# Kernel optimization log

Measured on AMD Instinct MI355X. Metric: run time of the kernel, lower is better.

The kernel has to match this reference:

```python
import jax, jax.numpy as jnp
import numpy as np

B, L, D = 32, 2048, 768
H = 512
EPS = 1e-5  # batch_norm eps (PyG MLP default norm)


def setup_inputs() -> dict:
    key = jax.random.key(0)
    ks = jax.random.split(key, 8)
    hidden = jax.random.normal(ks[0], (B, L, D), dtype=jnp.float32)
    attention_mask = jax.random.randint(ks[1], (B, L), 0, 2, dtype=jnp.int32)
    W1 = jax.random.normal(ks[2], (D, H), dtype=jnp.float32) * 0.02
    b1 = jnp.zeros((H,), dtype=jnp.float32)
    gamma = jnp.ones((H,), dtype=jnp.float32)
    beta = jnp.zeros((H,), dtype=jnp.float32)
    W2 = jax.random.normal(ks[3], (H, H), dtype=jnp.float32) * 0.02
    b2 = jnp.zeros((H,), dtype=jnp.float32)
    return {"hidden": hidden, "attention_mask": attention_mask,
            "W1": W1, "b1": b1, "gamma": gamma, "beta": beta,
            "W2": W2, "b2": b2}


def reference(hidden, attention_mask, W1, b1, gamma, beta, W2, b2):
    # Valid-token mask; pads are excluded from the batched graph's node set.
    m = attention_mask.astype(hidden.dtype)[..., None]  # (B, L, 1)
    n_valid = jnp.maximum(jnp.sum(m), 1.0)

    # MLP layer 1: Linear -> BatchNorm (stats over all valid nodes across the
    # whole batched graph, mirroring PyG MLP training-mode batch_norm) -> ReLU
    h = jnp.einsum('bld,dh->blh', hidden, W1) + b1  # (B, L, H)
    mean = jnp.sum(h * m, axis=(0, 1)) / n_valid
    var = jnp.sum(jnp.square(h - mean) * m, axis=(0, 1)) / n_valid
    h = (h - mean) * jax.lax.rsqrt(var + EPS) * gamma + beta
    h = jax.nn.relu(h)

    # MLP layer 2 (plain_last: no norm/act)
    out = jnp.einsum('blh,hk->blk', h, W2) + b2  # (B, L, H)

    # scores == ones -> segment softmax over each sequence's valid tokens is
    # uniform 1/n_b; scatter_add over batch ids == masked mean pool.
    counts = jnp.maximum(jnp.sum(m, axis=1), 1.0)  # (B, 1)
    pooled = jnp.sum(out * m, axis=1) / counts  # (B, H)
    return pooled
```

## Files before the change

### kernel.cpp

```cpp
#include <hip/hip_runtime.h>
#include <hip/hip_bf16.h>

#define Bn 32
#define Ln 2048
#define Dn 768
#define Hn 512
#define Mn (Bn*Ln)
#define EPSC 1e-5f

#define OFF_S1   0
#define OFF_S2   512
#define OFF_CNT  2048
#define OFF_PH   2304
#define OFF_W1T_BYTES  131072
#define OFF_H_BYTES    1048576

#define BM 128
#define BN2 256
#define BK 64
#define LDK 72

typedef __attribute__((ext_vector_type(8))) short bf16x8;
typedef __attribute__((ext_vector_type(4))) float f32x4;

static __device__ __forceinline__ unsigned short f2bf(float x) {
  __hip_bfloat16 h = __float2bfloat16(x);
  return *reinterpret_cast<unsigned short*>(&h);
}
static __device__ __forceinline__ float bf2f(unsigned short u) {
  return __uint_as_float(((unsigned int)u) << 16);
}

__global__ __launch_bounds__(256) void pre_kernel(const int* __restrict__ mask,
                                                  float* __restrict__ ws) {
  int blk = blockIdx.x, t = threadIdx.x;
  if (blk < Bn) {
    __shared__ int red[256];
    int s = 0;
#pragma unroll
    for (int i = 0; i < 8; i++) s += mask[blk * Ln + i * 256 + t];
    red[t] = s;
    __syncthreads();
    for (int off = 128; off > 0; off >>= 1) {
      if (t < off) red[t] += red[t + off];
      __syncthreads();
    }
    if (t == 0) ws[OFF_CNT + blk] = (float)red[0];
  } else {
#pragma unroll
    for (int i = 0; i < 4; i++) ws[OFF_S1 + i * 256 + t] = 0.f;
#pragma unroll
    for (int i = 0; i < 64; i++) ws[OFF_PH + i * 256 + t] = 0.f;
  }
}

__global__ __launch_bounds__(256) void transpose_w1(
    const float* __restrict__ W1, unsigned short* __restrict__ W1t) {
  __shared__ float tile[32][33];
  int kx = blockIdx.x * 32;
  int nx = blockIdx.y * 32;
  int tx = threadIdx.x & 31, ty = threadIdx.x >> 5;
#pragma unroll
  for (int i = 0; i < 32; i += 8)
    tile[ty + i][tx] = W1[(size_t)(kx + ty + i) * Hn + nx + tx];
  __syncthreads();
#pragma unroll
  for (int i = 0; i < 32; i += 8)
    W1t[(size_t)(nx + ty + i) * Dn + kx + tx] = f2bf(tile[tx][ty + i]);
}

__global__ __launch_bounds__(512, 4) void gemm1_mfma(
    const float* __restrict__ A, const unsigned short* __restrict__ W1t,
    const float* __restrict__ b1, const int* __restrict__ mask,
    unsigned short* __restrict__ Hout,
    float* __restrict__ gsum, float* __restrict__ gsq)
{
  __shared__ unsigned short As[BM * LDK];
  __shared__ unsigned short Bs[BN2 * LDK];
  __shared__ float csum[BN2];
  __shared__ float csq[BN2];

  const int t = threadIdx.x;
  const int bx = blockIdx.x;
  const int by = blockIdx.y;
  const int bm0 = by * BM;
  const int bn0 = bx * BN2;

  const int w = t >> 6;
  const int lane = t & 63;
  const int wm0 = (w >> 2) * 64;
  const int wn0 = (w & 3) * 64;
  const int l15 = lane & 15;
  const int quad = lane >> 4;

  const int am = t >> 2;
  const int ak = (t & 3) * 16;
  const int bn = t >> 1;
  const int bk = (t & 1) * 32;

  const float* Ap = A + (size_t)(bm0 + am) * Dn + ak;
  const unsigned short* Bp = W1t + (size_t)(bn0 + bn) * Dn + bk;

  f32x4 acc[4][4];
#pragma unroll
  for (int i = 0; i < 4; i++)
#pragma unroll
    for (int j = 0; j < 4; j++) acc[i][j] = (f32x4){0.f, 0.f, 0.f, 0.f};

  for (int k0 = 0; k0 < Dn; k0 += BK) {
    float4 a0 = *(const float4*)(Ap + k0);
    float4 a1 = *(const float4*)(Ap + k0 + 4);
    float4 a2 = *(const float4*)(Ap + k0 + 8);
    float4 a3 = *(const float4*)(Ap + k0 + 12);
    uint4 bv0 = *(const uint4*)(Bp + k0);
    uint4 bv1 = *(const uint4*)(Bp + k0 + 8);
    uint4 bv2 = *(const uint4*)(Bp + k0 + 16);
    uint4 bv3 = *(const uint4*)(Bp + k0 + 24);
    __syncthreads();
    uint4 p0, p1;
    p0.x = (unsigned int)f2bf(a0.x) | ((unsigned int)f2bf(a0.y) << 16);
    p0.y = (unsigned int)f2bf(a0.z) | ((unsigned int)f2bf(a0.w) << 16);
    p0.z = (unsigned int)f2bf(a1.x) | ((unsigned int)f2bf(a1.y) << 16);
    p0.w = (unsigned int)f2bf(a1.z) | ((unsigned int)f2bf(a1.w) << 16);
    p1.x = (unsigned int)f2bf(a2.x) | ((unsigned int)f2bf(a2.y) << 16);
    p1.y = (unsigned int)f2bf(a2.z) | ((unsigned int)f2bf(a2.w) << 16);
    p1.z = (unsigned int)f2bf(a3.x) | ((unsigned int)f2bf(a3.y) << 16);
    p1.w = (unsigned int)f2bf(a3.z) | ((unsigned int)f2bf(a3.w) << 16);
    *(uint4*)&As[am * LDK + ak] = p0;
    *(uint4*)&As[am * LDK + ak + 8] = p1;
    *(uint4*)&Bs[bn * LDK + bk] = bv0;
    *(uint4*)&Bs[bn * LDK + bk + 8] = bv1;
    *(uint4*)&Bs[bn * LDK + bk + 16] = bv2;
    *(uint4*)&Bs[bn * LDK + bk + 24] = bv3;
    __syncthreads();
#pragma unroll
    for (int s = 0; s < 2; s++) {
      bf16x8 af[4], bf[4];
#pragma unroll
      for (int mt = 0; mt < 4; mt++)
        af[mt] = *(const bf16x8*)&As[(wm0 + mt * 16 + l15) * LDK + s * 32 + quad * 8];
#pragma unroll
      for (int nt = 0; nt < 4; nt++)
        bf[nt] = *(const bf16x8*)&Bs[(wn0 + nt * 16 + l15) * LDK + s * 32 + quad * 8];
#pragma unroll
      for (int mt = 0; mt < 4; mt++)
#pragma unroll
        for (int nt = 0; nt < 4; nt++)
          acc[mt][nt] = __builtin_amdgcn_mfma_f32_16x16x32_bf16(
              af[mt], bf[nt], acc[mt][nt], 0, 0, 0);
    }
  }

  if (t < BN2) { csum[t] = 0.f; csq[t] = 0.f; }
  __syncthreads();

  float mk[4][4];
#pragma unroll
  for (int mt = 0; mt < 4; mt++) {
    int4 mv = *(const int4*)(mask + bm0 + wm0 + mt * 16 + quad * 4);
    mk[mt][0] = (float)mv.x; mk[mt][1] = (float)mv.y;
    mk[mt][2] = (float)mv.z; mk[mt][3] = (float)mv.w;
  }

  const size_t cbase = ((size_t)(by * 2 + bx)) * 32768 + (size_t)w * 4096;
#pragma unroll
  for (int nt = 0; nt < 4; nt++) {
    const int nl = wn0 + nt * 16 + l15;
    const float bias = b1[bn0 + nl];
    float ps = 0.f, pq = 0.f;
#pragma unroll
    for (int mt = 0; mt < 4; mt++) {
      ushort4 st;
      float v0 = acc[mt][nt][0] + bias;
      float v1 = acc[mt][nt][1] + bias;
      float v2 = acc[mt][nt][2] + bias;
      float v3 = acc[mt][nt][3] + bias;
      ps += v0 * mk[mt][0] + v1 * mk[mt][1] + v2 * mk[mt][2] + v3 * mk[mt][3];
      pq += v0 * v0 * mk[mt][0] + v1 * v1 * mk[mt][1] +
            v2 * v2 * mk[mt][2] + v3 * v3 * mk[mt][3];
      st.x = f2bf(v0); st.y = f2bf(v1); st.z = f2bf(v2); st.w = f2bf(v3);
      *(ushort4*)&Hout[cbase + (size_t)(mt * 4 + nt) * 256 + lane * 4] = st;
    }
    atomicAdd(&csum[nl], ps);
    atomicAdd(&csq[nl], pq);
  }

  __syncthreads();
  if (t < BN2) {
    atomicAdd(&gsum[bn0 + t], csum[t]);
    atomicAdd(&gsq[bn0 + t], csq[t]);
  }
}

__global__ __launch_bounds__(256) void bnpool_kernel(
    const unsigned short* __restrict__ Hbuf, const int* __restrict__ mask,
    const float* __restrict__ ws, const float* __restrict__ gamma,
    const float* __restrict__ beta, float* __restrict__ PH)
{
  __shared__ float mkf[BM];
  __shared__ float redc[32];
  const int t = threadIdx.x;
  const int chunk = blockIdx.x;
  const int by = chunk >> 1, bx = chunk & 1;
  const int b = chunk >> 5;
  if (t < 32) redc[t] = ws[OFF_CNT + t];
  if (t < BM) mkf[t] = (float)mask[by * BM + t];
  __syncthreads();

  float nv = 0.f;
#pragma unroll
  for (int i = 0; i < 32; i++) nv += redc[i];
  nv = fmaxf(nv, 1.f);
  const float inv = 1.f / nv;
  const int c = bx * BN2 + t;
  const float m = ws[OFF_S1 + c] * inv;
  const float var = ws[OFF_S2 + c] * inv - m * m;
  const float istd = rsqrtf(fmaxf(var, 0.f) + EPSC);
  const float scv = istd * gamma[c];
  const float shv = beta[c] - m * scv;

  const int w3 = t >> 6, nt = (t >> 4) & 3, l15 = t & 15;
  float acc = 0.f;
#pragma unroll
  for (int h = 0; h < 2; h++) {
    const int w = w3 + h * 4;
    const int wm0 = h * 64;
    const unsigned short* base =
        Hbuf + (size_t)chunk * 32768 + (size_t)w * 4096 + nt * 256 + l15 * 4;
#pragma unroll
    for (int mt = 0; mt < 4; mt++)
#pragma unroll
      for (int q = 0; q < 4; q++) {
        ushort4 hv = *(const ushort4*)(base + mt * 1024 + q * 64);
        const float* mv = &mkf[wm0 + mt * 16 + q * 4];
        acc += fmaxf(fmaf(bf2f(hv.x), scv, shv), 0.f) * mv[0]
             + fmaxf(fmaf(bf2f(hv.y), scv, shv), 0.f) * mv[1]
             + fmaxf(fmaf(bf2f(hv.z), scv, shv), 0.f) * mv[2]
             + fmaxf(fmaf(bf2f(hv.w), scv, shv), 0.f) * mv[3];
      }
  }
  atomicAdd(&PH[b * Hn + c], acc);
}

__global__ __launch_bounds__(128) void final_kernel(
    const float* __restrict__ pooledh, const float* __restrict__ cnt,
    const float* __restrict__ W2, const float* __restrict__ b2,
    float* __restrict__ out)
{
  __shared__ float pr[Hn];
  int b = blockIdx.x >> 2;
  int cc = blockIdx.x & 3;
  int t = threadIdx.x;
  float nb = cnt[b];
  float inv = 1.f / fmaxf(nb, 1.f);
#pragma unroll
  for (int i = 0; i < 4; i++)
    pr[t + i * 128] = pooledh[b * Hn + t + i * 128] * inv;
  __syncthreads();
  int c = cc * 128 + t;
  float a0 = 0.f, a1 = 0.f, a2 = 0.f, a3 = 0.f;
  for (int i = 0; i < Hn; i += 4) {
    a0 = fmaf(pr[i],     W2[(size_t)i * Hn + c],       a0);
    a1 = fmaf(pr[i + 1], W2[(size_t)(i + 1) * Hn + c], a1);
    a2 = fmaf(pr[i + 2], W2[(size_t)(i + 2) * Hn + c], a2);
    a3 = fmaf(pr[i + 3], W2[(size_t)(i + 3) * Hn + c], a3);
  }
  out[b * Hn + c] = (a0 + a1) + (a2 + a3) + b2[c] * (nb * inv);
}

extern "C" void kernel_launch(void* const* d_in, const int* in_sizes, int n_in,
                              void* d_out, int out_size, void* d_ws, size_t ws_size,
                              hipStream_t stream) {
  const float* hidden = (const float*)d_in[0];
  const int*   mask   = (const int*)d_in[1];
  const float* W1     = (const float*)d_in[2];
  const float* b1     = (const float*)d_in[3];
  const float* gamma  = (const float*)d_in[4];
  const float* beta   = (const float*)d_in[5];
  const float* W2     = (const float*)d_in[6];
  const float* b2     = (const float*)d_in[7];
  float* out = (float*)d_out;
  float* ws  = (float*)d_ws;
  unsigned short* W1t  = (unsigned short*)((char*)d_ws + OFF_W1T_BYTES);
  unsigned short* Hbuf = (unsigned short*)((char*)d_ws + OFF_H_BYTES);

  pre_kernel<<<Bn + 1, 256, 0, stream>>>(mask, ws);
  transpose_w1<<<dim3(Dn / 32, Hn / 32), 256, 0, stream>>>(W1, W1t);
  gemm1_mfma<<<dim3(Hn / BN2, Mn / BM), 512, 0, stream>>>(
      hidden, W1t, b1, mask, Hbuf, ws + OFF_S1, ws + OFF_S2);
  bnpool_kernel<<<(Mn / BM) * (Hn / BN2), 256, 0, stream>>>(
      Hbuf, mask, ws, gamma, beta, ws + OFF_PH);
  final_kernel<<<Bn * 4, 128, 0, stream>>>(ws + OFF_PH, ws + OFF_CNT, W2, b2, out);
}
```

Before: 390.2 us.

## Double-buffer gemm1 K loop with async LDS loads for W1 and swizzle

```diff
diff --git a/kernel.cpp b/kernel.cpp
--- a/kernel.cpp
+++ b/kernel.cpp
@@ -19,6 +19,7 @@
 #define BN2 256
 #define BK 64
 #define LDK 72
+#define KT_N (Dn/BK)
 
 typedef __attribute__((ext_vector_type(8))) short bf16x8;
 typedef __attribute__((ext_vector_type(4))) float f32x4;
@@ -69,14 +70,14 @@
     W1t[(size_t)(nx + ty + i) * Dn + kx + tx] = f2bf(tile[tx][ty + i]);
 }
 
-__global__ __launch_bounds__(512, 4) void gemm1_mfma(
+__global__ __launch_bounds__(512, 2) void gemm1_mfma(
     const float* __restrict__ A, const unsigned short* __restrict__ W1t,
     const float* __restrict__ b1, const int* __restrict__ mask,
     unsigned short* __restrict__ Hout,
     float* __restrict__ gsum, float* __restrict__ gsq)
 {
-  __shared__ unsigned short As[BM * LDK];
-  __shared__ unsigned short Bs[BN2 * LDK];
+  __shared__ __align__(16) unsigned short As3[2][BM * LDK];
+  __shared__ __align__(16) unsigned short Bs3[2][BN2 * BK];
   __shared__ float csum[BN2];
   __shared__ float csq[BN2];
 
@@ -95,11 +96,7 @@
 
   const int am = t >> 2;
   const int ak = (t & 3) * 16;
-  const int bn = t >> 1;
-  const int bk = (t & 1) * 32;
-
   const float* Ap = A + (size_t)(bm0 + am) * Dn + ak;
-  const unsigned short* Bp = W1t + (size_t)(bn0 + bn) * Dn + bk;
 
   f32x4 acc[4][4];
 #pragma unroll
@@ -107,49 +104,105 @@
 #pragma unroll
     for (int j = 0; j < 4; j++) acc[i][j] = (f32x4){0.f, 0.f, 0.f, 0.f};
 
-  for (int k0 = 0; k0 < Dn; k0 += BK) {
-    float4 a0 = *(const float4*)(Ap + k0);
-    float4 a1 = *(const float4*)(Ap + k0 + 4);
-    float4 a2 = *(const float4*)(Ap + k0 + 8);
-    float4 a3 = *(const float4*)(Ap + k0 + 12);
-    uint4 bv0 = *(const uint4*)(Bp + k0);
-    uint4 bv1 = *(const uint4*)(Bp + k0 + 8);
-    uint4 bv2 = *(const uint4*)(Bp + k0 + 16);
-    uint4 bv3 = *(const uint4*)(Bp + k0 + 24);
-    __syncthreads();
-    uint4 p0, p1;
-    p0.x = (unsigned int)f2bf(a0.x) | ((unsigned int)f2bf(a0.y) << 16);
-    p0.y = (unsigned int)f2bf(a0.z) | ((unsigned int)f2bf(a0.w) << 16);
-    p0.z = (unsigned int)f2bf(a1.x) | ((unsigned int)f2bf(a1.y) << 16);
-    p0.w = (unsigned int)f2bf(a1.z) | ((unsigned int)f2bf(a1.w) << 16);
-    p1.x = (unsigned int)f2bf(a2.x) | ((unsigned int)f2bf(a2.y) << 16);
-    p1.y = (unsigned int)f2bf(a2.z) | ((unsigned int)f2bf(a2.w) << 16);
-    p1.z = (unsigned int)f2bf(a3.x) | ((unsigned int)f2bf(a3.y) << 16);
-    p1.w = (unsigned int)f2bf(a3.z) | ((unsigned int)f2bf(a3.w) << 16);
-    *(uint4*)&As[am * LDK + ak] = p0;
-    *(uint4*)&As[am * LDK + ak + 8] = p1;
-    *(uint4*)&Bs[bn * LDK + bk] = bv0;
-    *(uint4*)&Bs[bn * LDK + bk + 8] = bv1;
-    *(uint4*)&Bs[bn * LDK + bk + 16] = bv2;
-    *(uint4*)&Bs[bn * LDK + bk + 24] = bv3;
-    __syncthreads();
-#pragma unroll
-    for (int s = 0; s < 2; s++) {
-      bf16x8 af[4], bf[4];
-#pragma unroll
-      for (int mt = 0; mt < 4; mt++)
-        af[mt] = *(const bf16x8*)&As[(wm0 + mt * 16 + l15) * LDK + s * 32 + quad * 8];
-#pragma unroll
-      for (int nt = 0; nt < 4; nt++)
-        bf[nt] = *(const bf16x8*)&Bs[(wn0 + nt * 16 + l15) * LDK + s * 32 + quad * 8];
-#pragma unroll
-      for (int mt = 0; mt < 4; mt++)
-#pragma unroll
-        for (int nt = 0; nt < 4; nt++)
-          acc[mt][nt] = __builtin_amdgcn_mfma_f32_16x16x32_bf16(
-              af[mt], bf[nt], acc[mt][nt], 0, 0, 0);
-    }
-  }
+  float4 rAe[4], rAo[4];
+
+#define WAITV(N) do { asm volatile("s_waitcnt vmcnt(" #N ")" ::: "memory"); \
+                      __builtin_amdgcn_sched_barrier(0); } while (0)
+#define WAITL0() do { asm volatile("s_waitcnt lgkmcnt(0)" ::: "memory"); \
+                      __builtin_amdgcn_sched_barrier(0); } while (0)
+
+#define STAGE_B(KT2, NS) do { \
+  _Pragma("unroll") \
+  for (int j = 0; j < 4; ++j) { \
+    const int p = ((w * 4 + j) << 10) + (lane << 4); \
+    const int q = p ^ (((p >> 7) & 7) << 4); \
+    const char* gsrc = (const char*)(W1t + (size_t)(bn0 + (q >> 7)) * Dn \
+                                     + (KT2) * BK) + (q & 127); \
+    __builtin_amdgcn_global_load_lds( \
+        (const __attribute__((address_space(1))) void*)gsrc, \
+        (__attribute__((address_space(3))) void*)((char*)&Bs3[NS][0] \
+                                                  + ((w * 4 + j) << 10)), \
+        16, 0, 0); \
+  } \
+} while (0)
+
+#define LOAD_A(KT, R) do { \
+  R[0] = *(const float4*)(Ap + (KT) * BK); \
+  R[1] = *(const float4*)(Ap + (KT) * BK + 4); \
+  R[2] = *(const float4*)(Ap + (KT) * BK + 8); \
+  R[3] = *(const float4*)(Ap + (KT) * BK + 12); \
+} while (0)
+
+#define PACK_WRITE(R, NS) do { \
+  uint4 p0, p1; \
+  p0.x = (unsigned)f2bf(R[0].x) | ((unsigned)f2bf(R[0].y) << 16); \
+  p0.y = (unsigned)f2bf(R[0].z) | ((unsigned)f2bf(R[0].w) << 16); \
+  p0.z = (unsigned)f2bf(R[1].x) | ((unsigned)f2bf(R[1].y) << 16); \
+  p0.w = (unsigned)f2bf(R[1].z) | ((unsigned)f2bf(R[1].w) << 16); \
+  p1.x = (unsigned)f2bf(R[2].x) | ((unsigned)f2bf(R[2].y) << 16); \
+  p1.y = (unsigned)f2bf(R[2].z) | ((unsigned)f2bf(R[2].w) << 16); \
+  p1.z = (unsigned)f2bf(R[3].x) | ((unsigned)f2bf(R[3].y) << 16); \
+  p1.w = (unsigned)f2bf(R[3].z) | ((unsigned)f2bf(R[3].w) << 16); \
+  *(uint4*)&As3[NS][am * LDK + ak] = p0; \
+  *(uint4*)&As3[NS][am * LDK + ak + 8] = p1; \
+} while (0)
+
+#define MFMA_ALL(CS) do { \
+  _Pragma("unroll") \
+  for (int s = 0; s < 2; ++s) { \
+    bf16x8 af[4], bf[4]; \
+    _Pragma("unroll") \
+    for (int mt = 0; mt < 4; ++mt) \
+      af[mt] = *(const bf16x8*)&As3[CS][(wm0 + mt * 16 + l15) * LDK \
+                                        + s * 32 + quad * 8]; \
+    _Pragma("unroll") \
+    for (int nt = 0; nt < 4; ++nt) { \
+      const int rb = wn0 + nt * 16 + l15; \
+      const int cb = (s * 64 + quad * 16) ^ ((rb & 7) << 4); \
+      bf[nt] = *(const bf16x8*)((const char*)&Bs3[CS][0] + rb * 128 + cb); \
+    } \
+    _Pragma("unroll") \
+    for (int mt = 0; mt < 4; ++mt) \
+      _Pragma("unroll") \
+      for (int nt = 0; nt < 4; ++nt) \
+        acc[mt][nt] = __builtin_amdgcn_mfma_f32_16x16x32_bf16( \
+            af[mt], bf[nt], acc[mt][nt], 0, 0, 0); \
+  } \
+} while (0)
+
+#define K_ITER(KT, CS, RL, RW) do { \
+  if ((KT) < KT_N - 1) STAGE_B((KT) + 1, (CS) ^ 1); \
+  __builtin_amdgcn_sched_barrier(0); \
+  if ((KT) < KT_N - 2) LOAD_A((KT) + 2, RL); \
+  if ((KT) < KT_N - 1) PACK_WRITE(RW, (CS) ^ 1); \
+  MFMA_ALL(CS); \
+  if ((KT) < KT_N - 2) { WAITV(4); } else { WAITV(0); } \
+  WAITL0(); \
+  __builtin_amdgcn_s_barrier(); \
+} while (0)
+
+  STAGE_B(0, 0);
+  __builtin_amdgcn_sched_barrier(0);
+  LOAD_A(0, rAe);
+  LOAD_A(1, rAo);
+  WAITV(0);
+  PACK_WRITE(rAe, 0);
+  WAITL0();
+  __builtin_amdgcn_s_barrier();
+
+#pragma unroll
+  for (int k2 = 0; k2 < KT_N / 2; ++k2) {
+    K_ITER(k2 * 2,     0, rAe, rAo);
+    K_ITER(k2 * 2 + 1, 1, rAo, rAe);
+  }
+
+#undef K_ITER
+#undef MFMA_ALL
+#undef PACK_WRITE
+#undef LOAD_A
+#undef STAGE_B
+#undef WAITL0
+#undef WAITV
 
   if (t < BN2) { csum[t] = 0.f; csq[t] = 0.f; }
   __syncthreads();
```

Measured after the change: 392.7 us. Within noise of the previous version (+0.6%).

## Fuse GEMM, batchnorm-pool and final projection into one cooperative persistent kernel

Applied to the files above, without the earlier changes.

```diff
diff --git a/kernel.cpp b/kernel.cpp
--- a/kernel.cpp
+++ b/kernel.cpp
@@ -1,5 +1,8 @@
 #include <hip/hip_runtime.h>
 #include <hip/hip_bf16.h>
+#include <hip/hip_cooperative_groups.h>
+
+namespace cg = cooperative_groups;
 
 #define Bn 32
 #define Ln 2048
@@ -13,12 +16,12 @@
 #define OFF_CNT  2048
 #define OFF_PH   2304
 #define OFF_W1T_BYTES  131072
-#define OFF_H_BYTES    1048576
 
 #define BM 128
 #define BN2 256
 #define BK 64
 #define LDK 72
+#define KT_N (Dn/BK)
 
 typedef __attribute__((ext_vector_type(8))) short bf16x8;
 typedef __attribute__((ext_vector_type(4))) float f32x4;
@@ -27,12 +30,10 @@
   __hip_bfloat16 h = __float2bfloat16(x);
   return *reinterpret_cast<unsigned short*>(&h);
 }
-static __device__ __forceinline__ float bf2f(unsigned short u) {
-  return __uint_as_float(((unsigned int)u) << 16);
-}
-
-__global__ __launch_bounds__(256) void pre_kernel(const int* __restrict__ mask,
-                                                  float* __restrict__ ws) {
+
+__global__ __launch_bounds__(256) void prep_kernel(
+    const int* __restrict__ mask, const float* __restrict__ W1,
+    unsigned short* __restrict__ W1t, float* __restrict__ ws) {
   int blk = blockIdx.x, t = threadIdx.x;
   if (blk < Bn) {
     __shared__ int red[256];
@@ -46,44 +47,44 @@
       __syncthreads();
     }
     if (t == 0) ws[OFF_CNT + blk] = (float)red[0];
+  } else if (blk == Bn) {
+#pragma unroll
+    for (int i = 0; i < 4; i++) ws[OFF_S1 + i * 256 + t] = 0.f;
+#pragma unroll
+    for (int i = 0; i < 64; i++) ws[OFF_PH + i * 256 + t] = 0.f;
   } else {
-#pragma unroll
-    for (int i = 0; i < 4; i++) ws[OFF_S1 + i * 256 + t] = 0.f;
-#pragma unroll
-    for (int i = 0; i < 64; i++) ws[OFF_PH + i * 256 + t] = 0.f;
+    __shared__ float tile[32][33];
+    int tb = blk - (Bn + 1);
+    int kx = (tb % 24) * 32;
+    int nx = (tb / 24) * 32;
+    int tx = t & 31, ty = t >> 5;
+#pragma unroll
+    for (int i = 0; i < 32; i += 8)
+      tile[ty + i][tx] = W1[(size_t)(kx + ty + i) * Hn + nx + tx];
+    __syncthreads();
+#pragma unroll
+    for (int i = 0; i < 32; i += 8)
+      W1t[(size_t)(nx + ty + i) * Dn + kx + tx] = f2bf(tile[tx][ty + i]);
   }
 }
 
-__global__ __launch_bounds__(256) void transpose_w1(
-    const float* __restrict__ W1, unsigned short* __restrict__ W1t) {
-  __shared__ float tile[32][33];
-  int kx = blockIdx.x * 32;
-  int nx = blockIdx.y * 32;
-  int tx = threadIdx.x & 31, ty = threadIdx.x >> 5;
-#pragma unroll
-  for (int i = 0; i < 32; i += 8)
-    tile[ty + i][tx] = W1[(size_t)(kx + ty + i) * Hn + nx + tx];
-  __syncthreads();
-#pragma unroll
-  for (int i = 0; i < 32; i += 8)
-    W1t[(size_t)(nx + ty + i) * Dn + kx + tx] = f2bf(tile[tx][ty + i]);
-}
-
-__global__ __launch_bounds__(512, 4) void gemm1_mfma(
+__global__ __launch_bounds__(512, 2) void fused_gemm_pool(
     const float* __restrict__ A, const unsigned short* __restrict__ W1t,
     const float* __restrict__ b1, const int* __restrict__ mask,
-    unsigned short* __restrict__ Hout,
-    float* __restrict__ gsum, float* __restrict__ gsq)
+    const float* __restrict__ gamma, const float* __restrict__ beta,
+    const float* __restrict__ W2, const float* __restrict__ b2,
+    float* __restrict__ ws, float* __restrict__ out)
 {
-  __shared__ unsigned short As[BM * LDK];
-  __shared__ unsigned short Bs[BN2 * LDK];
+  __shared__ __align__(16) unsigned short As[BM * LDK];
+  __shared__ __align__(16) unsigned short Bs[BN2 * BK];
   __shared__ float csum[BN2];
   __shared__ float csq[BN2];
+  __shared__ float pr[4][Hn];
 
   const int t = threadIdx.x;
-  const int bx = blockIdx.x;
-  const int by = blockIdx.y;
-  const int bm0 = by * BM;
+  const int bid = blockIdx.x;
+  const int bx = bid & 1;
+  const int my = bid >> 1;
   const int bn0 = bx * BN2;
 
   const int w = t >> 6;
@@ -95,177 +96,202 @@
 
   const int am = t >> 2;
   const int ak = (t & 3) * 16;
-  const int bn = t >> 1;
-  const int bk = (t & 1) * 32;
-
-  const float* Ap = A + (size_t)(bm0 + am) * Dn + ak;
-  const unsigned short* Bp = W1t + (size_t)(bn0 + bn) * Dn + bk;
-
-  f32x4 acc[4][4];
-#pragma unroll
-  for (int i = 0; i < 4; i++)
-#pragma unroll
-    for (int j = 0; j < 4; j++) acc[i][j] = (f32x4){0.f, 0.f, 0.f, 0.f};
-
-  for (int k0 = 0; k0 < Dn; k0 += BK) {
-    float4 a0 = *(const float4*)(Ap + k0);
-    float4 a1 = *(const float4*)(Ap + k0 + 4);
-    float4 a2 = *(const float4*)(Ap + k0 + 8);
-    float4 a3 = *(const float4*)(Ap + k0 + 12);
-    uint4 bv0 = *(const uint4*)(Bp + k0);
-    uint4 bv1 = *(const uint4*)(Bp + k0 + 8);
-    uint4 bv2 = *(const uint4*)(Bp + k0 + 16);
-    uint4 bv3 = *(const uint4*)(Bp + k0 + 24);
-    __syncthreads();
-    uint4 p0, p1;
-    p0.x = (unsigned int)f2bf(a0.x) | ((unsigned int)f2bf(a0.y) << 16);
-    p0.y = (unsigned int)f2bf(a0.z) | ((unsigned int)f2bf(a0.w) << 16);
-    p0.z = (unsigned int)f2bf(a1.x) | ((unsigned int)f2bf(a1.y) << 16);
-    p0.w = (unsigned int)f2bf(a1.z) | ((unsigned int)f2bf(a1.w) << 16);
-    p1.x = (unsigned int)f2bf(a2.x) | ((unsigned int)f2bf(a2.y) << 16);
-    p1.y = (unsigned int)f2bf(a2.z) | ((unsigned int)f2bf(a2.w) << 16);
-    p1.z = (unsigned int)f2bf(a3.x) | ((unsigned int)f2bf(a3.y) << 16);
-    p1.w = (unsigned int)f2bf(a3.z) | ((unsigned int)f2bf(a3.w) << 16);
-    *(uint4*)&As[am * LDK + ak] = p0;
-    *(uint4*)&As[am * LDK + ak + 8] = p1;
-    *(uint4*)&Bs[bn * LDK + bk] = bv0;
-    *(uint4*)&Bs[bn * LDK + bk + 8] = bv1;
-    *(uint4*)&Bs[bn * LDK + bk + 16] = bv2;
-    *(uint4*)&Bs[bn * LDK + bk + 24] = bv3;
-    __syncthreads();
-#pragma unroll
-    for (int s = 0; s < 2; s++) {
-      bf16x8 af[4], bf[4];
-#pragma unroll
-      for (int mt = 0; mt < 4; mt++)
-        af[mt] = *(const bf16x8*)&As[(wm0 + mt * 16 + l15) * LDK + s * 32 + quad * 8];
-#pragma unroll
-      for (int nt = 0; nt < 4; nt++)
-        bf[nt] = *(const bf16x8*)&Bs[(wn0 + nt * 16 + l15) * LDK + s * 32 + quad * 8];
-#pragma unroll
-      for (int mt = 0; mt < 4; mt++)
-#pragma unroll
-        for (int nt = 0; nt < 4; nt++)
-          acc[mt][nt] = __builtin_amdgcn_mfma_f32_16x16x32_bf16(
-              af[mt], bf[nt], acc[mt][nt], 0, 0, 0);
-    }
-  }
-
-  if (t < BN2) { csum[t] = 0.f; csq[t] = 0.f; }
-  __syncthreads();
-
-  float mk[4][4];
-#pragma unroll
-  for (int mt = 0; mt < 4; mt++) {
-    int4 mv = *(const int4*)(mask + bm0 + wm0 + mt * 16 + quad * 4);
-    mk[mt][0] = (float)mv.x; mk[mt][1] = (float)mv.y;
-    mk[mt][2] = (float)mv.z; mk[mt][3] = (float)mv.w;
-  }
-
-  const size_t cbase = ((size_t)(by * 2 + bx)) * 32768 + (size_t)w * 4096;
-#pragma unroll
-  for (int nt = 0; nt < 4; nt++) {
-    const int nl = wn0 + nt * 16 + l15;
-    const float bias = b1[bn0 + nl];
-    float ps = 0.f, pq = 0.f;
+
+  float* gsum = ws + OFF_S1;
+  float* gsq  = ws + OFF_S2;
+  float* PH   = ws + OFF_PH;
+
+  unsigned int hst[4][32];
+  unsigned int mb[4];
+
+#pragma unroll
+  for (int ci = 0; ci < 4; ++ci) {
+    const int tile = my + 128 * ci;
+    const int bm0 = tile * BM;
+    const float* Ap = A + (size_t)(bm0 + am) * Dn + ak;
+
+    f32x4 acc[4][4];
+#pragma unroll
+    for (int i = 0; i < 4; i++)
+#pragma unroll
+      for (int j = 0; j < 4; j++) acc[i][j] = (f32x4){0.f, 0.f, 0.f, 0.f};
+
+    for (int k0 = 0; k0 < KT_N; ++k0) {
+      float4 a0 = *(const float4*)(Ap + k0 * BK);
+      float4 a1 = *(const float4*)(Ap + k0 * BK + 4);
+      float4 a2 = *(const float4*)(Ap + k0 * BK + 8);
+      float4 a3 = *(const float4*)(Ap + k0 * BK + 12);
+      __syncthreads();
+#pragma unroll
+      for (int j = 0; j < 4; ++j) {
+        const int p = ((w * 4 + j) << 10) + (lane << 4);
+        const int q = p ^ (((p >> 7) & 7) << 4);
+        const char* gsrc = (const char*)(W1t + (size_t)(bn0 + (q >> 7)) * Dn
+                                         + k0 * BK) + (q & 127);
+        __builtin_amdgcn_global_load_lds(
+            (const __attribute__((address_space(1))) void*)gsrc,
+            (__attribute__((address_space(3))) void*)((char*)&Bs[0]
+                                                      + ((w * 4 + j) << 10)),
+            16, 0, 0);
+      }
+      uint4 p0, p1;
+      p0.x = (unsigned)f2bf(a0.x) | ((unsigned)f2bf(a0.y) << 16);
+      p0.y = (unsigned)f2bf(a0.z) | ((unsigned)f2bf(a0.w) << 16);
+      p0.z = (unsigned)f2bf(a1.x) | ((unsigned)f2bf(a1.y) << 16);
+      p0.w = (unsigned)f2bf(a1.z) | ((unsigned)f2bf(a1.w) << 16);
+      p1.x = (unsigned)f2bf(a2.x) | ((unsigned)f2bf(a2.y) << 16);
+      p1.y = (unsigned)f2bf(a2.z) | ((unsigned)f2bf(a2.w) << 16);
+      p1.z = (unsigned)f2bf(a3.x) | ((unsigned)f2bf(a3.y) << 16);
+      p1.w = (unsigned)f2bf(a3.z) | ((unsigned)f2bf(a3.w) << 16);
+      *(uint4*)&As[am * LDK + ak] = p0;
+      *(uint4*)&As[am * LDK + ak + 8] = p1;
+      __syncthreads();
+#pragma unroll
+      for (int s = 0; s < 2; ++s) {
+        bf16x8 af[4], bf[4];
+#pragma unroll
+        for (int mt = 0; mt < 4; ++mt)
+          af[mt] = *(const bf16x8*)&As[(wm0 + mt * 16 + l15) * LDK
+                                       + s * 32 + quad * 8];
+#pragma unroll
+        for (int nt = 0; nt < 4; ++nt) {
+          const int rb = wn0 + nt * 16 + l15;
+          const int cb = (s * 64 + quad * 16) ^ ((rb & 7) << 4);
+          bf[nt] = *(const bf16x8*)((const char*)&Bs[0] + rb * 128 + cb);
+        }
+#pragma unroll
+        for (int mt = 0; mt < 4; ++mt)
+#pragma unroll
+          for (int nt = 0; nt < 4; ++nt)
+            acc[mt][nt] = __builtin_amdgcn_mfma_f32_16x16x32_bf16(
+                af[mt], bf[nt], acc[mt][nt], 0, 0, 0);
+      }
+    }
+
+    unsigned int mbits = 0;
 #pragma unroll
     for (int mt = 0; mt < 4; mt++) {
-      ushort4 st;
-      float v0 = acc[mt][nt][0] + bias;
-      float v1 = acc[mt][nt][1] + bias;
-      float v2 = acc[mt][nt][2] + bias;
-      float v3 = acc[mt][nt][3] + bias;
-      ps += v0 * mk[mt][0] + v1 * mk[mt][1] + v2 * mk[mt][2] + v3 * mk[mt][3];
-      pq += v0 * v0 * mk[mt][0] + v1 * v1 * mk[mt][1] +
-            v2 * v2 * mk[mt][2] + v3 * v3 * mk[mt][3];
-      st.x = f2bf(v0); st.y = f2bf(v1); st.z = f2bf(v2); st.w = f2bf(v3);
-      *(ushort4*)&Hout[cbase + (size_t)(mt * 4 + nt) * 256 + lane * 4] = st;
-    }
-    atomicAdd(&csum[nl], ps);
-    atomicAdd(&csq[nl], pq);
-  }
-
-  __syncthreads();
-  if (t < BN2) {
-    atomicAdd(&gsum[bn0 + t], csum[t]);
-    atomicAdd(&gsq[bn0 + t], csq[t]);
-  }
-}
-
-__global__ __launch_bounds__(256) void bnpool_kernel(
-    const unsigned short* __restrict__ Hbuf, const int* __restrict__ mask,
-    const float* __restrict__ ws, const float* __restrict__ gamma,
-    const float* __restrict__ beta, float* __restrict__ PH)
-{
-  __shared__ float mkf[BM];
-  __shared__ float redc[32];
-  const int t = threadIdx.x;
-  const int chunk = blockIdx.x;
-  const int by = chunk >> 1, bx = chunk & 1;
-  const int b = chunk >> 5;
-  if (t < 32) redc[t] = ws[OFF_CNT + t];
-  if (t < BM) mkf[t] = (float)mask[by * BM + t];
-  __syncthreads();
+      int4 mv = *(const int4*)(mask + bm0 + wm0 + mt * 16 + quad * 4);
+      mbits |= (unsigned)(mv.x & 1) << (mt * 4);
+      mbits |= (unsigned)(mv.y & 1) << (mt * 4 + 1);
+      mbits |= (unsigned)(mv.z & 1) << (mt * 4 + 2);
+      mbits |= (unsigned)(mv.w & 1) << (mt * 4 + 3);
+    }
+    mb[ci] = mbits;
+
+    if (t < BN2) { csum[t] = 0.f; csq[t] = 0.f; }
+    __syncthreads();
+#pragma unroll
+    for (int nt = 0; nt < 4; nt++) {
+      const int nl = wn0 + nt * 16 + l15;
+      const float bias = b1[bn0 + nl];
+      float ps = 0.f, pq = 0.f;
+#pragma unroll
+      for (int mt = 0; mt < 4; mt++) {
+        float v0 = acc[mt][nt][0] + bias;
+        float v1 = acc[mt][nt][1] + bias;
+        float v2 = acc[mt][nt][2] + bias;
+        float v3 = acc[mt][nt][3] + bias;
+        float m0 = (float)((mbits >> (mt * 4)) & 1);
+        float m1 = (float)((mbits >> (mt * 4 + 1)) & 1);
+        float m2 = (float)((mbits >> (mt * 4 + 2)) & 1);
+        float m3 = (float)((mbits >> (mt * 4 + 3)) & 1);
+        ps += v0 * m0 + v1 * m1 + v2 * m2 + v3 * m3;
+        pq += v0 * v0 * m0 + v1 * v1 * m1 + v2 * v2 * m2 + v3 * v3 * m3;
+        hst[ci][nt * 8 + mt * 2]     =
+            (unsigned)f2bf(v0) | ((unsigned)f2bf(v1) << 16);
+        hst[ci][nt * 8 + mt * 2 + 1] =
+            (unsigned)f2bf(v2) | ((unsigned)f2bf(v3) << 16);
+      }
+      atomicAdd(&csum[nl], ps);
+      atomicAdd(&csq[nl], pq);
+    }
+    __syncthreads();
+    if (t < BN2) {
+      atomicAdd(&gsum[bn0 + t], csum[t]);
+      atomicAdd(&gsq[bn0 + t], csq[t]);
+    }
+  }
+
+  cg::this_grid().sync();
 
   float nv = 0.f;
 #pragma unroll
-  for (int i = 0; i < 32; i++) nv += redc[i];
+  for (int i = 0; i < Bn; i++) nv += ws[OFF_CNT + i];
   nv = fmaxf(nv, 1.f);
   const float inv = 1.f / nv;
-  const int c = bx * BN2 + t;
-  const float m = ws[OFF_S1 + c] * inv;
-  const float var = ws[OFF_S2 + c] * inv - m * m;
-  const float istd = rsqrtf(fmaxf(var, 0.f) + EPSC);
-  const float scv = istd * gamma[c];
-  const float shv = beta[c] - m * scv;
-
-  const int w3 = t >> 6, nt = (t >> 4) & 3, l15 = t & 15;
-  float acc = 0.f;
-#pragma unroll
-  for (int h = 0; h < 2; h++) {
-    const int w = w3 + h * 4;
-    const int wm0 = h * 64;
-    const unsigned short* base =
-        Hbuf + (size_t)chunk * 32768 + (size_t)w * 4096 + nt * 256 + l15 * 4;
-#pragma unroll
-    for (int mt = 0; mt < 4; mt++)
-#pragma unroll
-      for (int q = 0; q < 4; q++) {
-        ushort4 hv = *(const ushort4*)(base + mt * 1024 + q * 64);
-        const float* mv = &mkf[wm0 + mt * 16 + q * 4];
-        acc += fmaxf(fmaf(bf2f(hv.x), scv, shv), 0.f) * mv[0]
-             + fmaxf(fmaf(bf2f(hv.y), scv, shv), 0.f) * mv[1]
-             + fmaxf(fmaf(bf2f(hv.z), scv, shv), 0.f) * mv[2]
-             + fmaxf(fmaf(bf2f(hv.w), scv, shv), 0.f) * mv[3];
+  float scv[4], shv[4];
+#pragma unroll
+  for (int nt = 0; nt < 4; nt++) {
+    const int c = bn0 + wn0 + nt * 16 + l15;
+    const float mean = gsum[c] * inv;
+    const float var = gsq[c] * inv - mean * mean;
+    const float istd = rsqrtf(fmaxf(var, 0.f) + EPSC);
+    scv[nt] = istd * gamma[c];
+    shv[nt] = beta[c] - mean * scv[nt];
+  }
+
+#pragma unroll
+  for (int ci = 0; ci < 4; ++ci) {
+    __syncthreads();
+    if (t < BN2) csum[t] = 0.f;
+    __syncthreads();
+    const int b = (my + 128 * ci) >> 4;
+    const unsigned int mbits = mb[ci];
+#pragma unroll
+    for (int nt = 0; nt < 4; nt++) {
+      float accp = 0.f;
+#pragma unroll
+      for (int mt = 0; mt < 4; mt++) {
+        const unsigned u0 = hst[ci][nt * 8 + mt * 2];
+        const unsigned u1 = hst[ci][nt * 8 + mt * 2 + 1];
+        const float f0 = __uint_as_float(u0 << 16);
+        const float f1 = __uint_as_float(u0 & 0xFFFF0000u);
+        const float f2 = __uint_as_float(u1 << 16);
+        const float f3 = __uint_as_float(u1 & 0xFFFF0000u);
+        const float m0 = (float)((mbits >> (mt * 4)) & 1);
+        const float m1 = (float)((mbits >> (mt * 4 + 1)) & 1);
+        const float m2 = (float)((mbits >> (mt * 4 + 2)) & 1);
+        const float m3 = (float)((mbits >> (mt * 4 + 3)) & 1);
+        accp += fmaxf(fmaf(f0, scv[nt], shv[nt]), 0.f) * m0
+              + fmaxf(fmaf(f1, scv[nt], shv[nt]), 0.f) * m1
+              + fmaxf(fmaf(f2, scv[nt], shv[nt]), 0.f) * m2
+              + fmaxf(fmaf(f3, scv[nt], shv[nt]), 0.f) * m3;
       }
-  }
-  atomicAdd(&PH[b * Hn + c], acc);
-}
-
-__global__ __launch_bounds__(128) void final_kernel(
-    const float* __restrict__ pooledh, const float* __restrict__ cnt,
-    const float* __restrict__ W2, const float* __restrict__ b2,
-    float* __restrict__ out)
-{
-  __shared__ float pr[Hn];
-  int b = blockIdx.x >> 2;
-  int cc = blockIdx.x & 3;
-  int t = threadIdx.x;
-  float nb = cnt[b];
-  float inv = 1.f / fmaxf(nb, 1.f);
-#pragma unroll
-  for (int i = 0; i < 4; i++)
-    pr[t + i * 128] = pooledh[b * Hn + t + i * 128] * inv;
-  __syncthreads();
-  int c = cc * 128 + t;
-  float a0 = 0.f, a1 = 0.f, a2 = 0.f, a3 = 0.f;
-  for (int i = 0; i < Hn; i += 4) {
-    a0 = fmaf(pr[i],     W2[(size_t)i * Hn + c],       a0);
-    a1 = fmaf(pr[i + 1], W2[(size_t)(i + 1) * Hn + c], a1);
-    a2 = fmaf(pr[i + 2], W2[(size_t)(i + 2) * Hn + c], a2);
-    a3 = fmaf(pr[i + 3], W2[(size_t)(i + 3) * Hn + c], a3);
-  }
-  out[b * Hn + c] = (a0 + a1) + (a2 + a3) + b2[c] * (nb * inv);
+      atomicAdd(&csum[wn0 + nt * 16 + l15], accp);
+    }
+    __syncthreads();
+    if (t < BN2) atomicAdd(&PH[b * Hn + bn0 + t], csum[t]);
+  }
+
+  cg::this_grid().sync();
+
+  if (bid < 8) {
+    float nbq[4];
+#pragma unroll
+    for (int q = 0; q < 4; q++) {
+      const int bb = bid * 4 + q;
+      const float nb = ws[OFF_CNT + bb];
+      const float iv = 1.f / fmaxf(nb, 1.f);
+      pr[q][t] = PH[bb * Hn + t] * iv;
+      nbq[q] = nb * iv;
+    }
+    __syncthreads();
+    float o0 = 0.f, o1 = 0.f, o2 = 0.f, o3 = 0.f;
+    for (int k = 0; k < Hn; k += 2) {
+      const float wv0 = W2[(size_t)k * Hn + t];
+      const float wv1 = W2[(size_t)(k + 1) * Hn + t];
+      o0 = fmaf(pr[0][k], wv0, fmaf(pr[0][k + 1], wv1, o0));
+      o1 = fmaf(pr[1][k], wv0, fmaf(pr[1][k + 1], wv1, o1));
+      o2 = fmaf(pr[2][k], wv0, fmaf(pr[2][k + 1], wv1, o2));
+      o3 = fmaf(pr[3][k], wv0, fmaf(pr[3][k + 1], wv1, o3));
+    }
+    const float bb2 = b2[t];
+    out[(size_t)(bid * 4 + 0) * Hn + t] = o0 + bb2 * nbq[0];
+    out[(size_t)(bid * 4 + 1) * Hn + t] = o1 + bb2 * nbq[1];
+    out[(size_t)(bid * 4 + 2) * Hn + t] = o2 + bb2 * nbq[2];
+    out[(size_t)(bid * 4 + 3) * Hn + t] = o3 + bb2 * nbq[3];
+  }
 }
 
 extern "C" void kernel_launch(void* const* d_in, const int* in_sizes, int n_in,
@@ -281,14 +307,14 @@
   const float* b2     = (const float*)d_in[7];
   float* out = (float*)d_out;
   float* ws  = (float*)d_ws;
-  unsigned short* W1t  = (unsigned short*)((char*)d_ws + OFF_W1T_BYTES);
-  unsigned short* Hbuf = (unsigned short*)((char*)d_ws + OFF_H_BYTES);
-
-  pre_kernel<<<Bn + 1, 256, 0, stream>>>(mask, ws);
-  transpose_w1<<<dim3(Dn / 32, Hn / 32), 256, 0, stream>>>(W1, W1t);
-  gemm1_mfma<<<dim3(Hn / BN2, Mn / BM), 512, 0, stream>>>(
-      hidden, W1t, b1, mask, Hbuf, ws + OFF_S1, ws + OFF_S2);
-  bnpool_kernel<<<(Mn / BM) * (Hn / BN2), 256, 0, stream>>>(
-      Hbuf, mask, ws, gamma, beta, ws + OFF_PH);
-  final_kernel<<<Bn * 4, 128, 0, stream>>>(ws + OFF_PH, ws + OFF_CNT, W2, b2, out);
+  unsigned short* W1t = (unsigned short*)((char*)d_ws + OFF_W1T_BYTES);
+
+  prep_kernel<<<Bn + 1 + (Dn / 32) * (Hn / 32), 256, 0, stream>>>(
+      mask, W1, W1t, ws);
+
+  void* kargs[] = {(void*)&hidden, (void*)&W1t, (void*)&b1, (void*)&mask,
+                   (void*)&gamma, (void*)&beta, (void*)&W2, (void*)&b2,
+                   (void*)&ws, (void*)&out};
+  hipLaunchCooperativeKernel((const void*)fused_gemm_pool, dim3(256),
+                             dim3(512), kargs, 0, stream);
 }
```

Result: slower. 499.6 us (+28.0%).

## Replace LDS-staged GEMM1 with direct-from-global MFMA fragment loads

Applied to the files above, without the earlier changes.

```diff
diff --git a/kernel.cpp b/kernel.cpp
--- a/kernel.cpp
+++ b/kernel.cpp
@@ -14,11 +14,6 @@
 #define OFF_PH   2304
 #define OFF_W1T_BYTES  131072
 #define OFF_H_BYTES    1048576
-
-#define BM 128
-#define BN2 256
-#define BK 64
-#define LDK 72
 
 typedef __attribute__((ext_vector_type(8))) short bf16x8;
 typedef __attribute__((ext_vector_type(4))) float f32x4;
@@ -69,37 +64,34 @@
     W1t[(size_t)(nx + ty + i) * Dn + kx + tx] = f2bf(tile[tx][ty + i]);
 }
 
-__global__ __launch_bounds__(512, 4) void gemm1_mfma(
+__global__ __launch_bounds__(256, 2) void gemm1_direct(
     const float* __restrict__ A, const unsigned short* __restrict__ W1t,
     const float* __restrict__ b1, const int* __restrict__ mask,
     unsigned short* __restrict__ Hout,
     float* __restrict__ gsum, float* __restrict__ gsq)
 {
-  __shared__ unsigned short As[BM * LDK];
-  __shared__ unsigned short Bs[BN2 * LDK];
-  __shared__ float csum[BN2];
-  __shared__ float csq[BN2];
+  __shared__ float csum[256];
+  __shared__ float csq[256];
 
   const int t = threadIdx.x;
   const int bx = blockIdx.x;
-  const int by = blockIdx.y;
-  const int bm0 = by * BM;
-  const int bn0 = bx * BN2;
-
+  const int by2 = blockIdx.y;
   const int w = t >> 6;
   const int lane = t & 63;
-  const int wm0 = (w >> 2) * 64;
-  const int wn0 = (w & 3) * 64;
   const int l15 = lane & 15;
   const int quad = lane >> 4;
 
-  const int am = t >> 2;
-  const int ak = (t & 3) * 16;
-  const int bn = t >> 1;
-  const int bk = (t & 1) * 32;
-
-  const float* Ap = A + (size_t)(bm0 + am) * Dn + ak;
-  const unsigned short* Bp = W1t + (size_t)(bn0 + bn) * Dn + bk;
+  const int row0 = by2 * 64;
+  const int col0 = bx * 256 + w * 64;
+
+  const float* Ap0 = A + (size_t)(row0 +  0 + l15) * Dn + quad * 8;
+  const float* Ap1 = A + (size_t)(row0 + 16 + l15) * Dn + quad * 8;
+  const float* Ap2 = A + (size_t)(row0 + 32 + l15) * Dn + quad * 8;
+  const float* Ap3 = A + (size_t)(row0 + 48 + l15) * Dn + quad * 8;
+  const unsigned short* Bp0 = W1t + (size_t)(col0 +  0 + l15) * Dn + quad * 8;
+  const unsigned short* Bp1 = W1t + (size_t)(col0 + 16 + l15) * Dn + quad * 8;
+  const unsigned short* Bp2 = W1t + (size_t)(col0 + 32 + l15) * Dn + quad * 8;
+  const unsigned short* Bp3 = W1t + (size_t)(col0 + 48 + l15) * Dn + quad * 8;
 
   f32x4 acc[4][4];
 #pragma unroll
@@ -107,66 +99,71 @@
 #pragma unroll
     for (int j = 0; j < 4; j++) acc[i][j] = (f32x4){0.f, 0.f, 0.f, 0.f};
 
-  for (int k0 = 0; k0 < Dn; k0 += BK) {
-    float4 a0 = *(const float4*)(Ap + k0);
-    float4 a1 = *(const float4*)(Ap + k0 + 4);
-    float4 a2 = *(const float4*)(Ap + k0 + 8);
-    float4 a3 = *(const float4*)(Ap + k0 + 12);
-    uint4 bv0 = *(const uint4*)(Bp + k0);
-    uint4 bv1 = *(const uint4*)(Bp + k0 + 8);
-    uint4 bv2 = *(const uint4*)(Bp + k0 + 16);
-    uint4 bv3 = *(const uint4*)(Bp + k0 + 24);
-    __syncthreads();
-    uint4 p0, p1;
-    p0.x = (unsigned int)f2bf(a0.x) | ((unsigned int)f2bf(a0.y) << 16);
-    p0.y = (unsigned int)f2bf(a0.z) | ((unsigned int)f2bf(a0.w) << 16);
-    p0.z = (unsigned int)f2bf(a1.x) | ((unsigned int)f2bf(a1.y) << 16);
-    p0.w = (unsigned int)f2bf(a1.z) | ((unsigned int)f2bf(a1.w) << 16);
-    p1.x = (unsigned int)f2bf(a2.x) | ((unsigned int)f2bf(a2.y) << 16);
-    p1.y = (unsigned int)f2bf(a2.z) | ((unsigned int)f2bf(a2.w) << 16);
-    p1.z = (unsigned int)f2bf(a3.x) | ((unsigned int)f2bf(a3.y) << 16);
-    p1.w = (unsigned int)f2bf(a3.z) | ((unsigned int)f2bf(a3.w) << 16);
-    *(uint4*)&As[am * LDK + ak] = p0;
-    *(uint4*)&As[am * LDK + ak + 8] = p1;
-    *(uint4*)&Bs[bn * LDK + bk] = bv0;
-    *(uint4*)&Bs[bn * LDK + bk + 8] = bv1;
-    *(uint4*)&Bs[bn * LDK + bk + 16] = bv2;
-    *(uint4*)&Bs[bn * LDK + bk + 24] = bv3;
-    __syncthreads();
-#pragma unroll
-    for (int s = 0; s < 2; s++) {
-      bf16x8 af[4], bf[4];
-#pragma unroll
-      for (int mt = 0; mt < 4; mt++)
-        af[mt] = *(const bf16x8*)&As[(wm0 + mt * 16 + l15) * LDK + s * 32 + quad * 8];
-#pragma unroll
-      for (int nt = 0; nt < 4; nt++)
-        bf[nt] = *(const bf16x8*)&Bs[(wn0 + nt * 16 + l15) * LDK + s * 32 + quad * 8];
-#pragma unroll
-      for (int mt = 0; mt < 4; mt++)
-#pragma unroll
-        for (int nt = 0; nt < 4; nt++)
-          acc[mt][nt] = __builtin_amdgcn_mfma_f32_16x16x32_bf16(
-              af[mt], bf[nt], acc[mt][nt], 0, 0, 0);
-    }
-  }
-
-  if (t < BN2) { csum[t] = 0.f; csq[t] = 0.f; }
+#define CVT8(AF, LO, HI) do { \
+  AF[0] = (short)f2bf((LO).x); AF[1] = (short)f2bf((LO).y); \
+  AF[2] = (short)f2bf((LO).z); AF[3] = (short)f2bf((LO).w); \
+  AF[4] = (short)f2bf((HI).x); AF[5] = (short)f2bf((HI).y); \
+  AF[6] = (short)f2bf((HI).z); AF[7] = (short)f2bf((HI).w); \
+} while (0)
+
+#pragma unroll
+  for (int k0 = 0; k0 < Dn; k0 += 32) {
+    bf16x8 bf0 = *(const bf16x8*)(Bp0 + k0);
+    bf16x8 bf1 = *(const bf16x8*)(Bp1 + k0);
+    bf16x8 bf2 = *(const bf16x8*)(Bp2 + k0);
+    bf16x8 bf3 = *(const bf16x8*)(Bp3 + k0);
+
+    float4 a0l = *(const float4*)(Ap0 + k0);
+    float4 a0h = *(const float4*)(Ap0 + k0 + 4);
+    float4 a1l = *(const float4*)(Ap1 + k0);
+    float4 a1h = *(const float4*)(Ap1 + k0 + 4);
+    float4 a2l = *(const float4*)(Ap2 + k0);
+    float4 a2h = *(const float4*)(Ap2 + k0 + 4);
+    float4 a3l = *(const float4*)(Ap3 + k0);
+    float4 a3h = *(const float4*)(Ap3 + k0 + 4);
+
+    bf16x8 af0, af1, af2, af3;
+    CVT8(af0, a0l, a0h);
+    CVT8(af1, a1l, a1h);
+    CVT8(af2, a2l, a2h);
+    CVT8(af3, a3l, a3h);
+
+    acc[0][0] = __builtin_amdgcn_mfma_f32_16x16x32_bf16(af0, bf0, acc[0][0], 0, 0, 0);
+    acc[0][1] = __builtin_amdgcn_mfma_f32_16x16x32_bf16(af0, bf1, acc[0][1], 0, 0, 0);
+    acc[0][2] = __builtin_amdgcn_mfma_f32_16x16x32_bf16(af0, bf2, acc[0][2], 0, 0, 0);
+    acc[0][3] = __builtin_amdgcn_mfma_f32_16x16x32_bf16(af0, bf3, acc[0][3], 0, 0, 0);
+    acc[1][0] = __builtin_amdgcn_mfma_f32_16x16x32_bf16(af1, bf0, acc[1][0], 0, 0, 0);
+    acc[1][1] = __builtin_amdgcn_mfma_f32_16x16x32_bf16(af1, bf1, acc[1][1], 0, 0, 0);
+    acc[1][2] = __builtin_amdgcn_mfma_f32_16x16x32_bf16(af1, bf2, acc[1][2], 0, 0, 0);
+    acc[1][3] = __builtin_amdgcn_mfma_f32_16x16x32_bf16(af1, bf3, acc[1][3], 0, 0, 0);
+    acc[2][0] = __builtin_amdgcn_mfma_f32_16x16x32_bf16(af2, bf0, acc[2][0], 0, 0, 0);
+    acc[2][1] = __builtin_amdgcn_mfma_f32_16x16x32_bf16(af2, bf1, acc[2][1], 0, 0, 0);
+    acc[2][2] = __builtin_amdgcn_mfma_f32_16x16x32_bf16(af2, bf2, acc[2][2], 0, 0, 0);
+    acc[2][3] = __builtin_amdgcn_mfma_f32_16x16x32_bf16(af2, bf3, acc[2][3], 0, 0, 0);
+    acc[3][0] = __builtin_amdgcn_mfma_f32_16x16x32_bf16(af3, bf0, acc[3][0], 0, 0, 0);
+    acc[3][1] = __builtin_amdgcn_mfma_f32_16x16x32_bf16(af3, bf1, acc[3][1], 0, 0, 0);
+    acc[3][2] = __builtin_amdgcn_mfma_f32_16x16x32_bf16(af3, bf2, acc[3][2], 0, 0, 0);
+    acc[3][3] = __builtin_amdgcn_mfma_f32_16x16x32_bf16(af3, bf3, acc[3][3], 0, 0, 0);
+  }
+#undef CVT8
+
+  csum[t] = 0.f;
+  csq[t] = 0.f;
   __syncthreads();
 
   float mk[4][4];
 #pragma unroll
   for (int mt = 0; mt < 4; mt++) {
-    int4 mv = *(const int4*)(mask + bm0 + wm0 + mt * 16 + quad * 4);
+    int4 mv = *(const int4*)(mask + row0 + mt * 16 + quad * 4);
     mk[mt][0] = (float)mv.x; mk[mt][1] = (float)mv.y;
     mk[mt][2] = (float)mv.z; mk[mt][3] = (float)mv.w;
   }
 
-  const size_t cbase = ((size_t)(by * 2 + bx)) * 32768 + (size_t)w * 4096;
+  const size_t cbase = (size_t)by2 * 32768 + (size_t)(bx * 4 + w) * 4096;
 #pragma unroll
   for (int nt = 0; nt < 4; nt++) {
-    const int nl = wn0 + nt * 16 + l15;
-    const float bias = b1[bn0 + nl];
+    const int nl = w * 64 + nt * 16 + l15;
+    const float bias = b1[bx * 256 + nl];
     float ps = 0.f, pq = 0.f;
 #pragma unroll
     for (int mt = 0; mt < 4; mt++) {
@@ -186,25 +183,22 @@
   }
 
   __syncthreads();
-  if (t < BN2) {
-    atomicAdd(&gsum[bn0 + t], csum[t]);
-    atomicAdd(&gsq[bn0 + t], csq[t]);
-  }
-}
-
-__global__ __launch_bounds__(256) void bnpool_kernel(
+  atomicAdd(&gsum[bx * 256 + t], csum[t]);
+  atomicAdd(&gsq[bx * 256 + t], csq[t]);
+}
+
+__global__ __launch_bounds__(512) void bnpool_kernel(
     const unsigned short* __restrict__ Hbuf, const int* __restrict__ mask,
     const float* __restrict__ ws, const float* __restrict__ gamma,
     const float* __restrict__ beta, float* __restrict__ PH)
 {
-  __shared__ float mkf[BM];
+  __shared__ float mkf[64];
   __shared__ float redc[32];
   const int t = threadIdx.x;
   const int chunk = blockIdx.x;
-  const int by = chunk >> 1, bx = chunk & 1;
   const int b = chunk >> 5;
   if (t < 32) redc[t] = ws[OFF_CNT + t];
-  if (t < BM) mkf[t] = (float)mask[by * BM + t];
+  if (t < 64) mkf[t] = (float)mask[chunk * 64 + t];
   __syncthreads();
 
   float nv = 0.f;
@@ -212,33 +206,28 @@
   for (int i = 0; i < 32; i++) nv += redc[i];
   nv = fmaxf(nv, 1.f);
   const float inv = 1.f / nv;
-  const int c = bx * BN2 + t;
+  const int c = t;
   const float m = ws[OFF_S1 + c] * inv;
   const float var = ws[OFF_S2 + c] * inv - m * m;
   const float istd = rsqrtf(fmaxf(var, 0.f) + EPSC);
   const float scv = istd * gamma[c];
   const float shv = beta[c] - m * scv;
 
-  const int w3 = t >> 6, nt = (t >> 4) & 3, l15 = t & 15;
+  const int wc = t >> 6, nt = (t >> 4) & 3, l15 = t & 15;
+  const unsigned short* base =
+      Hbuf + (size_t)chunk * 32768 + (size_t)wc * 4096 + nt * 256 + l15 * 4;
   float acc = 0.f;
 #pragma unroll
-  for (int h = 0; h < 2; h++) {
-    const int w = w3 + h * 4;
-    const int wm0 = h * 64;
-    const unsigned short* base =
-        Hbuf + (size_t)chunk * 32768 + (size_t)w * 4096 + nt * 256 + l15 * 4;
-#pragma unroll
-    for (int mt = 0; mt < 4; mt++)
-#pragma unroll
-      for (int q = 0; q < 4; q++) {
-        ushort4 hv = *(const ushort4*)(base + mt * 1024 + q * 64);
-        const float* mv = &mkf[wm0 + mt * 16 + q * 4];
-        acc += fmaxf(fmaf(bf2f(hv.x), scv, shv), 0.f) * mv[0]
-             + fmaxf(fmaf(bf2f(hv.y), scv, shv), 0.f) * mv[1]
-             + fmaxf(fmaf(bf2f(hv.z), scv, shv), 0.f) * mv[2]
-             + fmaxf(fmaf(bf2f(hv.w), scv, shv), 0.f) * mv[3];
-      }
-  }
+  for (int mt = 0; mt < 4; mt++)
+#pragma unroll
+    for (int q = 0; q < 4; q++) {
+      ushort4 hv = *(const ushort4*)(base + mt * 1024 + q * 64);
+      const float* mv = &mkf[mt * 16 + q * 4];
+      acc += fmaxf(fmaf(bf2f(hv.x), scv, shv), 0.f) * mv[0]
+           + fmaxf(fmaf(bf2f(hv.y), scv, shv), 0.f) * mv[1]
+           + fmaxf(fmaf(bf2f(hv.z), scv, shv), 0.f) * mv[2]
+           + fmaxf(fmaf(bf2f(hv.w), scv, shv), 0.f) * mv[3];
+    }
   atomicAdd(&PH[b * Hn + c], acc);
 }
 
@@ -286,9 +275,9 @@
 
   pre_kernel<<<Bn + 1, 256, 0, stream>>>(mask, ws);
   transpose_w1<<<dim3(Dn / 32, Hn / 32), 256, 0, stream>>>(W1, W1t);
-  gemm1_mfma<<<dim3(Hn / BN2, Mn / BM), 512, 0, stream>>>(
+  gemm1_direct<<<dim3(2, Mn / 64), 256, 0, stream>>>(
       hidden, W1t, b1, mask, Hbuf, ws + OFF_S1, ws + OFF_S2);
-  bnpool_kernel<<<(Mn / BM) * (Hn / BN2), 256, 0, stream>>>(
+  bnpool_kernel<<<Mn / 64, 512, 0, stream>>>(
       Hbuf, mask, ws, gamma, beta, ws + OFF_PH);
   final_kernel<<<Bn * 4, 128, 0, stream>>>(ws + OFF_PH, ws + OFF_CNT, W2, b2, out);
 }
```

New measurement: 571.5 us. 46.4% more time.
